# Performance work log

Measured on AMD Instinct MI355X. Metric: run time of the kernel, lower is better.

The kernel has to match this reference:

```python
import jax, jax.numpy as jnp
import numpy as np

N_HEAD = 16
ROPE_BASE = 10000.0


def apply_rope(x):
    # x: [B, T, H, D], torchtune interleaved-pair RoPE
    B, T, H, D = x.shape
    pos = jnp.arange(T, dtype=jnp.float32)
    freqs = 1.0 / (ROPE_BASE ** (jnp.arange(0, D, 2, dtype=jnp.float32) / D))  # [D/2]
    theta = pos[:, None] * freqs[None, :]            # [T, D/2]
    cos = jnp.cos(theta)[None, :, None, :]           # [1, T, 1, D/2]
    sin = jnp.sin(theta)[None, :, None, :]
    xp = x.reshape(B, T, H, D // 2, 2)
    x0, x1 = xp[..., 0], xp[..., 1]
    out = jnp.stack([x0 * cos - x1 * sin, x1 * cos + x0 * sin], axis=-1)
    return out.reshape(B, T, H, D).astype(x.dtype)


def setup_inputs() -> dict:
    key = jax.random.key(0)
    k1, k2, k3 = jax.random.split(key, 3)
    B, T, C = 4, 2048, 1024
    x = jax.random.normal(k1, (B, T, C), dtype=jnp.float32)
    w_qkv = jax.random.normal(k2, (C, 3 * C), dtype=jnp.float32) * 0.02
    b_qkv = jnp.zeros((3 * C,), dtype=jnp.float32)
    w_proj = jax.random.normal(k3, (C, C), dtype=jnp.float32) * 0.02
    b_proj = jnp.zeros((C,), dtype=jnp.float32)
    return {"x": x, "w_qkv": w_qkv, "b_qkv": b_qkv, "w_proj": w_proj, "b_proj": b_proj}


def reference(x, w_qkv, b_qkv, w_proj, b_proj):
    B, T, C = x.shape
    H = N_HEAD
    D = C // H
    qkv = x @ w_qkv + b_qkv                          # [B, T, 3C]
    q, k, v = jnp.split(qkv, 3, axis=-1)
    q = apply_rope(q.reshape(B, T, H, D))
    k = apply_rope(k.reshape(B, T, H, D))
    v = v.reshape(B, T, H, D)
    scale = 1.0 / jnp.sqrt(jnp.asarray(D, dtype=x.dtype))
    attn = jnp.einsum('bthd,bshd->bhts', q, k) * scale  # [B, H, T, T] (non-causal)
    attn = jax.nn.softmax(attn, axis=-1)
    out = jnp.einsum('bhts,bshd->bthd', attn, v).reshape(B, T, C)
    return out @ w_proj + b_proj
```

## Files before the change

### kernel.cpp

```cpp
#include <hip/hip_runtime.h>

typedef unsigned short ushort_t;
typedef unsigned int   uint_t;
typedef __attribute__((ext_vector_type(8))) short bf16x8;
typedef __attribute__((ext_vector_type(4))) float f32x4;

__device__ __forceinline__ ushort_t f2bf(float f) {
    union { float f; uint_t i; } x; x.f = f;
    uint_t i = x.i + 0x7fffu + ((x.i >> 16) & 1u);
    return (ushort_t)(i >> 16);
}
__device__ __forceinline__ uint_t fbits(float f) {
    union { float f; uint_t i; } x; x.f = f;
    return x.i;
}
__device__ __forceinline__ void async16(const void* g, void* l) {
    __builtin_amdgcn_global_load_lds(
        (const __attribute__((address_space(1))) uint_t*)g,
        (__attribute__((address_space(3))) uint_t*)l, 16, 0, 0);
}

__global__ __launch_bounds__(256) void conv_bf16(
    const float* __restrict__ in, ushort_t* __restrict__ outp)
{
    int i = (blockIdx.x * 256 + threadIdx.x) * 4;
    float4 v = *(const float4*)(in + i);
    uint_t a = (uint_t)f2bf(v.x) | ((uint_t)f2bf(v.y) << 16);
    uint_t b = (uint_t)f2bf(v.z) | ((uint_t)f2bf(v.w) << 16);
    uint2 st = { a, b };
    *(uint2*)(outp + i) = st;
}

__global__ __launch_bounds__(256) void transpose_conv(
    const float* __restrict__ in, ushort_t* __restrict__ outp, int R, int C)
{
    __shared__ ushort_t t[64][65];
    int r0 = blockIdx.y * 64, c0 = blockIdx.x * 64;
    int lr = threadIdx.x >> 4, lc = (threadIdx.x & 15) * 4;
#pragma unroll
    for (int rr = 0; rr < 4; ++rr) {
        float4 v = *(const float4*)(in + (size_t)(r0 + rr * 16 + lr) * C + c0 + lc);
        t[lc + 0][rr * 16 + lr] = f2bf(v.x);
        t[lc + 1][rr * 16 + lr] = f2bf(v.y);
        t[lc + 2][rr * 16 + lr] = f2bf(v.z);
        t[lc + 3][rr * 16 + lr] = f2bf(v.w);
    }
    __syncthreads();
    int oc = threadIdx.x >> 2, och = (threadIdx.x & 3) * 16;
    union { uint4 v[2]; ushort_t u[16]; } pk;
#pragma unroll
    for (int j = 0; j < 16; ++j) pk.u[j] = t[oc][och + j];
    uint4* dst = (uint4*)(outp + (size_t)(c0 + oc) * R + r0 + och);
    dst[0] = pk.v[0]; dst[1] = pk.v[1];
}

__global__ __launch_bounds__(256) void rope_table_k(float2* __restrict__ tab)
{
    int idx = blockIdx.x * 256 + threadIdx.x;
    int t = idx >> 5, i = idx & 31;
    float freq = powf(10000.0f, -(float)i * (1.0f / 32.0f));
    float sn, cs;
    sincosf((float)t * freq, &sn, &cs);
    tab[idx] = make_float2(cs, sn);
}

template <int MODE>
__global__ __launch_bounds__(256) void gemm_mfma(
    const ushort_t* __restrict__ A, const ushort_t* __restrict__ Bt,
    const float* __restrict__ bias, void* __restrict__ Cv,
    const float2* __restrict__ tab, int M, int N, int K, int coloff)
{
    __shared__ ushort_t As[128][64];
    __shared__ ushort_t Bs[128][64];
    const int tid = threadIdx.x;
    const int w = tid >> 6, lane = tid & 63, ln = lane & 15, quad = lane >> 4;
    const int wm = w >> 1, wn = w & 1;

    const int lin = blockIdx.y * gridDim.x + blockIdx.x;
    const int per = (gridDim.x * gridDim.y) >> 3;
    const int nid = (lin & 7) * per + (lin >> 3);
    const int bx = nid % gridDim.x, by = nid / gridDim.x;
    const int row0 = by * 128, col0 = bx * 128 + coloff;

    f32x4 acc[4][4] = {};

    const int swch = (lane & 7) ^ (lane >> 3);
    const ushort_t* ga = A  + (size_t)(row0 + w * 8 + (lane >> 3)) * K + swch * 8;
    const ushort_t* gb = Bt + (size_t)(col0 + w * 8 + (lane >> 3)) * K + swch * 8;
    ushort_t* la = &As[w * 8][0];
    ushort_t* lb = &Bs[w * 8][0];
    const int rch0 = ln & 7;

    for (int k0 = 0; k0 < K; k0 += 64) {
#pragma unroll
        for (int j = 0; j < 4; ++j) {
            async16(ga + (size_t)(j * 32) * K + k0, la + j * 32 * 64);
            async16(gb + (size_t)(j * 32) * K + k0, lb + j * 32 * 64);
        }
        __syncthreads();
#pragma unroll
        for (int kk = 0; kk < 2; ++kk) {
            int ch = ((kk * 4 + quad) ^ rch0) * 8;
            bf16x8 af[4], bfv[4];
#pragma unroll
            for (int mt = 0; mt < 4; ++mt)
                af[mt] = *(const bf16x8*)&As[wm * 64 + mt * 16 + ln][ch];
#pragma unroll
            for (int nt = 0; nt < 4; ++nt)
                bfv[nt] = *(const bf16x8*)&Bs[wn * 64 + nt * 16 + ln][ch];
#pragma unroll
            for (int mt = 0; mt < 4; ++mt)
#pragma unroll
                for (int nt = 0; nt < 4; ++nt) {
                    if (MODE == 2)
                        acc[mt][nt] = __builtin_amdgcn_mfma_f32_16x16x32_bf16(
                            af[mt], bfv[nt], acc[mt][nt], 0, 0, 0);
                    else
                        acc[mt][nt] = __builtin_amdgcn_mfma_f32_16x16x32_bf16(
                            bfv[nt], af[mt], acc[mt][nt], 0, 0, 0);
                }
        }
        __syncthreads();
    }

    if (MODE == 2) {
#pragma unroll
        for (int nt = 0; nt < 4; ++nt) {
            int c = col0 + wn * 64 + nt * 16 + ln;
            float bv = bias[c];
            int c2 = c - 2048;
            size_t vrow = ((size_t)(c2 >> 6)) * 64 + (c2 & 63);
#pragma unroll
            for (int mt = 0; mt < 4; ++mt) {
                int rr = row0 + wm * 64 + mt * 16 + quad * 4;
                int b = rr >> 11, t0 = rr & 2047;
                uint2 st;
                st.x = (uint_t)f2bf(acc[mt][nt][0] + bv)
                     | ((uint_t)f2bf(acc[mt][nt][1] + bv) << 16);
                st.y = (uint_t)f2bf(acc[mt][nt][2] + bv)
                     | ((uint_t)f2bf(acc[mt][nt][3] + bv) << 16);
                *(uint2*)((ushort_t*)Cv + ((size_t)b * 16 * 64 + vrow) * 2048 + t0) = st;
            }
        }
    } else {
#pragma unroll
        for (int mt = 0; mt < 4; ++mt) {
            int rr = row0 + wm * 64 + mt * 16 + ln;
#pragma unroll
            for (int nt = 0; nt < 4; ++nt) {
                int c0 = col0 + wn * 64 + nt * 16 + quad * 4;
                float4 bv = *(const float4*)(bias + c0);
                float v0 = acc[mt][nt][0] + bv.x, v1 = acc[mt][nt][1] + bv.y;
                float v2 = acc[mt][nt][2] + bv.z, v3 = acc[mt][nt][3] + bv.w;
                if (MODE == 1) {
                    int i0 = (c0 & 63) >> 1;
                    const float2* trow = tab + (size_t)(rr & 2047) * 32;
                    float2 cs0 = trow[i0], cs1 = trow[i0 + 1];
                    float o0 = v0 * cs0.x - v1 * cs0.y;
                    float o1 = v1 * cs0.x + v0 * cs0.y;
                    float o2 = v2 * cs1.x - v3 * cs1.y;
                    float o3 = v3 * cs1.x + v2 * cs1.y;
                    uint2 st;
                    st.x = (uint_t)f2bf(o0) | ((uint_t)f2bf(o1) << 16);
                    st.y = (uint_t)f2bf(o2) | ((uint_t)f2bf(o3) << 16);
                    *(uint2*)((ushort_t*)Cv + (size_t)rr * N + c0) = st;
                } else {
                    float4 st = { v0, v1, v2, v3 };
                    *(float4*)((float*)Cv + (size_t)rr * N + c0) = st;
                }
            }
        }
    }
}

template <int MODE>
__global__ __launch_bounds__(512, 2) void gemm256(
    const ushort_t* __restrict__ A, const ushort_t* __restrict__ Bt,
    const float* __restrict__ bias, void* __restrict__ Cv,
    const float2* __restrict__ tab, int N)
{
    __shared__ ushort_t As[2][256][64];
    __shared__ ushort_t Bs[2][256][64];

    const int tid = threadIdx.x;
    const int w = tid >> 6, lane = tid & 63, ln = lane & 15, quad = lane >> 4;
    const int wm = w >> 2, wn = w & 3;

    const int lin = blockIdx.y * gridDim.x + blockIdx.x;
    const int per = (gridDim.x * gridDim.y) >> 3;
    const int nid = (lin & 7) * per + (lin >> 3);
    const int bx = nid % gridDim.x, by = nid / gridDim.x;
    const int row0 = by * 256, col0 = bx * 256;

    const int r6 = tid >> 3, c8 = tid & 7;
    const int swch = c8 ^ (r6 & 7);
    const ushort_t* ga = A  + (size_t)(row0 + r6) * 1024 + swch * 8;
    const ushort_t* gb = Bt + (size_t)(col0 + r6) * 1024 + swch * 8;
    ushort_t* lau = &As[0][0][0] + tid * 8;
    ushort_t* lbu = &Bs[0][0][0] + tid * 8;
    const int rch0 = ln & 7;

    f32x4 acc[8][4] = {};

#pragma unroll
    for (int j = 0; j < 4; ++j) {
        async16(ga + (size_t)(j * 64) * 1024, lau + j * 4096);
        async16(gb + (size_t)(j * 64) * 1024, lbu + j * 4096);
    }
    asm volatile("s_waitcnt vmcnt(0)" ::: "memory");
    __builtin_amdgcn_s_barrier();

#pragma unroll 2
    for (int k = 0; k < 16; ++k) {
        const int cur = k & 1;
        const int kn = (k < 15) ? k + 1 : k;
        const size_t koff = (size_t)kn * 64;
#pragma unroll
        for (int j = 0; j < 4; ++j) {
            async16(ga + (size_t)(j * 64) * 1024 + koff, lau + (cur ^ 1) * 16384 + j * 4096);
            async16(gb + (size_t)(j * 64) * 1024 + koff, lbu + (cur ^ 1) * 16384 + j * 4096);
        }
        bf16x8 bf[4];
#pragma unroll
        for (int q = 0; q < 4; ++q) {
            const int kk = q >> 1, mh = q & 1;
            const int ch = ((kk * 4 + quad) ^ rch0) * 8;
            if (mh == 0) {
#pragma unroll
                for (int nt = 0; nt < 4; ++nt)
                    bf[nt] = *(const bf16x8*)&Bs[cur][wn * 64 + nt * 16 + ln][ch];
            }
            bf16x8 af[4];
#pragma unroll
            for (int mt = 0; mt < 4; ++mt)
                af[mt] = *(const bf16x8*)&As[cur][mh * 128 + wm * 64 + mt * 16 + ln][ch];
            __builtin_amdgcn_s_setprio(1);
#pragma unroll
            for (int mt = 0; mt < 4; ++mt)
#pragma unroll
                for (int nt = 0; nt < 4; ++nt)
                    acc[mh * 4 + mt][nt] = __builtin_amdgcn_mfma_f32_16x16x32_bf16(
                        bf[nt], af[mt], acc[mh * 4 + mt][nt], 0, 0, 0);
            __builtin_amdgcn_s_setprio(0);
            if (q == 3)
                asm volatile("s_waitcnt vmcnt(0)" ::: "memory");
            __builtin_amdgcn_s_barrier();
        }
    }

#pragma unroll
    for (int mg = 0; mg < 8; ++mg) {
        const int rr = row0 + (mg >> 2) * 128 + wm * 64 + (mg & 3) * 16 + ln;
        const float2* trow = tab + (size_t)(rr & 2047) * 32;
#pragma unroll
        for (int nt = 0; nt < 4; ++nt) {
            const int c0 = col0 + wn * 64 + nt * 16 + quad * 4;
            float4 bv = *(const float4*)(bias + c0);
            float v0 = acc[mg][nt][0] + bv.x, v1 = acc[mg][nt][1] + bv.y;
            float v2 = acc[mg][nt][2] + bv.z, v3 = acc[mg][nt][3] + bv.w;
            if (MODE == 1) {
                const int i0 = (c0 & 63) >> 1;
                float2 cs0 = trow[i0], cs1 = trow[i0 + 1];
                float o0 = v0 * cs0.x - v1 * cs0.y;
                float o1 = v1 * cs0.x + v0 * cs0.y;
                float o2 = v2 * cs1.x - v3 * cs1.y;
                float o3 = v3 * cs1.x + v2 * cs1.y;
                uint2 st;
                st.x = (uint_t)f2bf(o0) | ((uint_t)f2bf(o1) << 16);
                st.y = (uint_t)f2bf(o2) | ((uint_t)f2bf(o3) << 16);
                *(uint2*)((ushort_t*)Cv + (size_t)rr * N + c0) = st;
            } else {
                float4 st = { v0, v1, v2, v3 };
                *(float4*)((float*)Cv + (size_t)rr * N + c0) = st;
            }
        }
    }
}

__global__ __launch_bounds__(512, 4) void attn_mfma(
    const ushort_t* __restrict__ qkv, const ushort_t* __restrict__ vtg,
    ushort_t* __restrict__ outp)
{
    __shared__ ushort_t Ks[2][64][64];
    __shared__ ushort_t Vts[2][64][64];
    __shared__ ushort_t Ps[8][16][72];

    const int tid = threadIdx.x;
    const int w = tid >> 6, lane = tid & 63, ln = lane & 15, quad = lane >> 4;
    const int bh = blockIdx.x, qt = blockIdx.y, b = bh >> 4, h = bh & 15;
    const size_t base = (size_t)b * 2048 * 3072 + h * 64;

    bf16x8 af[2][2];
#pragma unroll
    for (int s = 0; s < 2; ++s)
#pragma unroll
        for (int kk = 0; kk < 2; ++kk)
            af[s][kk] = *(const bf16x8*)(qkv + base
                + (size_t)(qt * 256 + w * 32 + s * 16 + ln) * 3072 + kk * 32 + quad * 8);

    bf16x8 ones;
#pragma unroll
    for (int j = 0; j < 8; ++j) ones[j] = (short)0x3F80;

    f32x4 oaccT[2][4] = {};
    f32x4 oneacc[2] = {};
    const float SC = 0.125f * 1.44269504f;

    const int swch = (lane & 7) ^ (lane >> 3);
    const ushort_t* kg = qkv + base + 1024 + (size_t)(lane >> 3) * 3072 + swch * 8;
    const ushort_t* vg = vtg + ((size_t)bh * 64 + (lane >> 3)) * 2048 + swch * 8;
    const int rch0 = ln & 7;
    const int r8 = w * 8;

    async16(kg + (size_t)r8 * 3072, &Ks[0][r8][0]);
    async16(vg + (size_t)r8 * 2048, &Vts[0][r8][0]);
    asm volatile("s_waitcnt vmcnt(0)" ::: "memory");
    __builtin_amdgcn_s_barrier();

    int cur = 0;
    for (int kt = 0; kt < 32; ++kt) {
        if (kt < 31) {
            async16(kg + (size_t)((kt + 1) * 64 + r8) * 3072, &Ks[cur ^ 1][r8][0]);
            async16(vg + (size_t)r8 * 2048 + (kt + 1) * 64, &Vts[cur ^ 1][r8][0]);
        }

        bf16x8 kf[2][4], vf[2][4];
#pragma unroll
        for (int kk = 0; kk < 2; ++kk) {
            int ch = ((kk * 4 + quad) ^ rch0) * 8;
#pragma unroll
            for (int nt = 0; nt < 4; ++nt) {
                kf[kk][nt] = *(const bf16x8*)&Ks[cur][nt * 16 + ln][ch];
                vf[kk][nt] = *(const bf16x8*)&Vts[cur][nt * 16 + ln][ch];
            }
        }

#pragma unroll
        for (int s = 0; s < 2; ++s) {
            f32x4 sacc[4] = {};
#pragma unroll
            for (int kk = 0; kk < 2; ++kk)
#pragma unroll
                for (int nt = 0; nt < 4; ++nt)
                    sacc[nt] = __builtin_amdgcn_mfma_f32_16x16x32_bf16(
                        kf[kk][nt], af[s][kk], sacc[nt], 0, 0, 0);

            if (s == 1)
                asm volatile("s_waitcnt lgkmcnt(0)" ::: "memory");
#pragma unroll
            for (int nt = 0; nt < 4; ++nt) {
                float e0 = __builtin_amdgcn_exp2f(fmaf(sacc[nt][0], SC, -24.0f));
                float e1 = __builtin_amdgcn_exp2f(fmaf(sacc[nt][1], SC, -24.0f));
                float e2 = __builtin_amdgcn_exp2f(fmaf(sacc[nt][2], SC, -24.0f));
                float e3 = __builtin_amdgcn_exp2f(fmaf(sacc[nt][3], SC, -24.0f));
                uint2 pk;
                pk.x = __builtin_amdgcn_perm(fbits(e1), fbits(e0), 0x07060302u);
                pk.y = __builtin_amdgcn_perm(fbits(e3), fbits(e2), 0x07060302u);
                *(uint2*)&Ps[w][ln][nt * 16 + quad * 4] = pk;
            }
            asm volatile("s_waitcnt lgkmcnt(0)" ::: "memory");

#pragma unroll
            for (int kk = 0; kk < 2; ++kk) {
                bf16x8 pf = *(const bf16x8*)&Ps[w][ln][kk * 32 + quad * 8];
                oneacc[s] = __builtin_amdgcn_mfma_f32_16x16x32_bf16(
                    ones, pf, oneacc[s], 0, 0, 0);
#pragma unroll
                for (int nt = 0; nt < 4; ++nt)
                    oaccT[s][nt] = __builtin_amdgcn_mfma_f32_16x16x32_bf16(
                        vf[kk][nt], pf, oaccT[s][nt], 0, 0, 0);
            }
        }

        asm volatile("s_waitcnt vmcnt(0) lgkmcnt(0)" ::: "memory");
        __builtin_amdgcn_s_barrier();
        cur ^= 1;
    }

#pragma unroll
    for (int s = 0; s < 2; ++s) {
        float linv = 1.0f / oneacc[s][0];
        size_t row = (size_t)b * 2048 + qt * 256 + w * 32 + s * 16 + ln;
#pragma unroll
        for (int nt = 0; nt < 4; ++nt) {
            uint2 st;
            st.x = (uint_t)f2bf(oaccT[s][nt][0] * linv)
                 | ((uint_t)f2bf(oaccT[s][nt][1] * linv) << 16);
            st.y = (uint_t)f2bf(oaccT[s][nt][2] * linv)
                 | ((uint_t)f2bf(oaccT[s][nt][3] * linv) << 16);
            *(uint2*)(outp + row * 1024 + h * 64 + nt * 16 + quad * 4) = st;
        }
    }
}

extern "C" void kernel_launch(void* const* d_in, const int* in_sizes, int n_in,
                              void* d_out, int out_size, void* d_ws, size_t ws_size,
                              hipStream_t stream)
{
    (void)in_sizes; (void)n_in; (void)out_size; (void)ws_size;

    const float* x      = (const float*)d_in[0];
    const float* w_qkv  = (const float*)d_in[1];
    const float* b_qkv  = (const float*)d_in[2];
    const float* w_proj = (const float*)d_in[3];
    const float* b_proj = (const float*)d_in[4];
    float*       out    = (float*)d_out;

    ushort_t* x_bf    = (ushort_t*)d_ws;
    ushort_t* wqkvT   = x_bf    + (size_t)8192 * 1024;
    ushort_t* wprojT  = wqkvT   + (size_t)3072 * 1024;
    ushort_t* qkv_bf  = wprojT  + (size_t)1024 * 1024;
    ushort_t* attn_bf = qkv_bf  + (size_t)8192 * 3072;
    ushort_t* vtg     = attn_bf + (size_t)8192 * 1024;
    float2*   tab     = (float2*)(vtg + (size_t)64 * 64 * 2048);

    conv_bf16<<<8192, 256, 0, stream>>>(x, x_bf);
    transpose_conv<<<dim3(48, 16), 256, 0, stream>>>(w_qkv, wqkvT, 1024, 3072);
    transpose_conv<<<dim3(16, 16), 256, 0, stream>>>(w_proj, wprojT, 1024, 1024);
    rope_table_k<<<256, 256, 0, stream>>>(tab);

    gemm256<1><<<dim3(8, 32), 512, 0, stream>>>(
        x_bf, wqkvT, b_qkv, qkv_bf, tab, 3072);

    gemm_mfma<2><<<dim3(8, 64), 256, 0, stream>>>(
        x_bf, wqkvT, b_qkv, vtg, nullptr, 8192, 3072, 1024, 2048);

    attn_mfma<<<dim3(64, 8), 512, 0, stream>>>(qkv_bf, vtg, attn_bf);

    gemm256<0><<<dim3(4, 32), 512, 0, stream>>>(
        attn_bf, wprojT, b_proj, out, nullptr, 1024);
}
```

Before: 290.5 us.

## Add dedicated 256x128-tile projection GEMM with swizzled LDS and block remap

Replaces the generic 256-wide gemm256 used for the output projection with a specialized kernel using 256x128 tiles. The grid grows from 128 to 256 blocks so more of the CUs get work. The kernel double-buffers its LDS with async global-to-LDS loads, XOR-swizzles LDS chunks to avoid bank conflicts, and remaps block IDs to improve L2 locality. The cost is less operand reuse per tile and hardcoded dimensions (K=1024, N=1024).

```diff
diff --git a/kernel.cpp b/kernel.cpp
--- a/kernel.cpp
+++ b/kernel.cpp
@@ -277,6 +277,90 @@
     }
 }
 
+__global__ __launch_bounds__(512, 2) void gemm_proj(
+    const ushort_t* __restrict__ A, const ushort_t* __restrict__ Bt,
+    const float* __restrict__ bias, float* __restrict__ C)
+{
+    __shared__ ushort_t As[2][256][64];
+    __shared__ ushort_t Bs[2][128][64];
+
+    const int tid = threadIdx.x;
+    const int w = tid >> 6, lane = tid & 63, ln = lane & 15, quad = lane >> 4;
+    const int wm = w >> 1, wn = w & 1;
+
+    const int lin = blockIdx.y * 8 + blockIdx.x;
+    const int nid = (lin & 7) * 32 + (lin >> 3);
+    const int bx = nid & 7, by = nid >> 3;
+    const int row0 = by * 256, col0 = bx * 128;
+
+    const int r6 = tid >> 3, c8 = tid & 7;
+    const int swch = c8 ^ (r6 & 7);
+    const ushort_t* ga = A  + (size_t)(row0 + r6) * 1024 + swch * 8;
+    const ushort_t* gb = Bt + (size_t)(col0 + r6) * 1024 + swch * 8;
+    ushort_t* lau = &As[0][0][0] + tid * 8;
+    ushort_t* lbu = &Bs[0][0][0] + tid * 8;
+    const int rch0 = ln & 7;
+
+    f32x4 acc[4][4] = {};
+
+#pragma unroll
+    for (int j = 0; j < 4; ++j)
+        async16(ga + (size_t)(j * 64) * 1024, lau + j * 4096);
+#pragma unroll
+    for (int j = 0; j < 2; ++j)
+        async16(gb + (size_t)(j * 64) * 1024, lbu + j * 4096);
+    asm volatile("s_waitcnt vmcnt(0)" ::: "memory");
+    __builtin_amdgcn_s_barrier();
+
+#pragma unroll 2
+    for (int k = 0; k < 16; ++k) {
+        const int cur = k & 1;
+        const int kn = (k < 15) ? k + 1 : k;
+        const size_t koff = (size_t)kn * 64;
+#pragma unroll
+        for (int j = 0; j < 4; ++j)
+            async16(ga + (size_t)(j * 64) * 1024 + koff, lau + (cur ^ 1) * 16384 + j * 4096);
+#pragma unroll
+        for (int j = 0; j < 2; ++j)
+            async16(gb + (size_t)(j * 64) * 1024 + koff, lbu + (cur ^ 1) * 8192 + j * 4096);
+#pragma unroll
+        for (int kk = 0; kk < 2; ++kk) {
+            const int ch = ((kk * 4 + quad) ^ rch0) * 8;
+            bf16x8 bf[4], af[4];
+#pragma unroll
+            for (int nt = 0; nt < 4; ++nt)
+                bf[nt] = *(const bf16x8*)&Bs[cur][wn * 64 + nt * 16 + ln][ch];
+#pragma unroll
+            for (int mt = 0; mt < 4; ++mt)
+                af[mt] = *(const bf16x8*)&As[cur][wm * 64 + mt * 16 + ln][ch];
+            __builtin_amdgcn_s_setprio(1);
+#pragma unroll
+            for (int mt = 0; mt < 4; ++mt)
+#pragma unroll
+                for (int nt = 0; nt < 4; ++nt)
+                    acc[mt][nt] = __builtin_amdgcn_mfma_f32_16x16x32_bf16(
+                        bf[nt], af[mt], acc[mt][nt], 0, 0, 0);
+            __builtin_amdgcn_s_setprio(0);
+            if (kk == 1)
+                asm volatile("s_waitcnt vmcnt(0)" ::: "memory");
+            __builtin_amdgcn_s_barrier();
+        }
+    }
+
+#pragma unroll
+    for (int mt = 0; mt < 4; ++mt) {
+        const int rr = row0 + wm * 64 + mt * 16 + ln;
+#pragma unroll
+        for (int nt = 0; nt < 4; ++nt) {
+            const int c0 = col0 + wn * 64 + nt * 16 + quad * 4;
+            float4 bv = *(const float4*)(bias + c0);
+            float4 st = { acc[mt][nt][0] + bv.x, acc[mt][nt][1] + bv.y,
+                          acc[mt][nt][2] + bv.z, acc[mt][nt][3] + bv.w };
+            *(float4*)(C + (size_t)rr * 1024 + c0) = st;
+        }
+    }
+}
+
 __global__ __launch_bounds__(512, 4) void attn_mfma(
     const ushort_t* __restrict__ qkv, const ushort_t* __restrict__ vtg,
     ushort_t* __restrict__ outp)
@@ -427,6 +511,5 @@
 
     attn_mfma<<<dim3(64, 8), 512, 0, stream>>>(qkv_bf, vtg, attn_bf);
 
-    gemm256<0><<<dim3(4, 32), 512, 0, stream>>>(
-        attn_bf, wprojT, b_proj, out, nullptr, 1024);
-}
+    gemm_proj<<<dim3(8, 32), 512, 0, stream>>>(attn_bf, wprojT, b_proj, out);
+}
```

New measurement: 278.9 us (median of 2 runs). -4.0%, faster.
